# Optimization experiments

Measured on AMD Instinct MI355X. Metric: run time of the kernel, lower is better.

The kernel has to match this reference:

```python
import math
import jax, jax.numpy as jnp
import numpy as np

DIM = 2048
HID = 4 * DIM
SEQ = 2048
BATCH = 2
EPS = 1e-5


def _layernorm(x, g, b):
    mu = jnp.mean(x, axis=-1, keepdims=True)
    var = jnp.var(x, axis=-1, keepdims=True)
    return (x - mu) * jax.lax.rsqrt(var + EPS) * g + b


def setup_inputs() -> dict:
    key = jax.random.key(0)
    ks = jax.random.split(key, 12)
    s = 1.0 / math.sqrt(DIM)
    x = jax.random.normal(ks[0], (BATCH, SEQ, DIM), dtype=jnp.float32)
    # additive causal mask: 0 on/below diagonal, -1e9 above
    mask = jnp.where(jnp.tril(jnp.ones((SEQ, SEQ), dtype=bool)), 0.0, -1e9).astype(jnp.float32)
    freqs_cis = jax.random.normal(ks[1], (SEQ, 64), dtype=jnp.float32)  # unused by forward
    return {
        "x": x,
        "mask": mask,
        "start_pos": 0,
        "freqs_cis": freqs_cis,
        "wq": jax.random.normal(ks[2], (DIM, DIM), dtype=jnp.float32) * s,
        "bq": jnp.zeros((DIM,), dtype=jnp.float32),
        "wk": jax.random.normal(ks[3], (DIM, DIM), dtype=jnp.float32) * s,
        "bk": jnp.zeros((DIM,), dtype=jnp.float32),
        "wv": jax.random.normal(ks[4], (DIM, DIM), dtype=jnp.float32) * s,
        "bv": jnp.zeros((DIM,), dtype=jnp.float32),
        "g_ln1": jnp.ones((DIM,), dtype=jnp.float32),
        "b_ln1": jnp.zeros((DIM,), dtype=jnp.float32),
        "g_ln2": jnp.ones((DIM,), dtype=jnp.float32),
        "b_ln2": jnp.zeros((DIM,), dtype=jnp.float32),
        "w1": jax.random.normal(ks[5], (DIM, HID), dtype=jnp.float32) * s,
        "b1": jnp.zeros((HID,), dtype=jnp.float32),
        "w2": jax.random.normal(ks[6], (HID, DIM), dtype=jnp.float32) * (1.0 / math.sqrt(HID)),
        "b2": jnp.zeros((DIM,), dtype=jnp.float32),
    }


def reference(x, mask, start_pos, freqs_cis, wq, bq, wk, bk, wv, bv,
              g_ln1, b_ln1, g_ln2, b_ln2, w1, b1, w2, b2):
    # pre-norm attention (no head split; scale by sqrt(full dim); dropout=eval identity)
    h = _layernorm(x, g_ln1, b_ln1)
    q = h @ wq + bq
    k = h @ wk + bk
    v = h @ wv + bv
    scores = jnp.einsum('bqd,bkd->bqk', q, k) / math.sqrt(DIM) + mask
    attn = jax.nn.softmax(scores, axis=-1)
    attn_out = jnp.einsum('bqk,bkd->bqd', attn, v)
    h2 = _layernorm(x + attn_out, g_ln2, b_ln2)
    ffn = jax.nn.gelu(h2 @ w1 + b1, approximate=False) @ w2 + b2
    # NOTE: original code adds FFN output to the ORIGINAL x (attn residual dropped here)
    return x + ffn
```

## Files before the change

### kernel.cpp

```cpp
#include <hip/hip_runtime.h>
#include <math.h>

#define DIM_ 2048
#define HID_ 8192
#define SEQ_ 2048
#define BATCH_ 2
#define TOK_ (BATCH_*SEQ_)

typedef __attribute__((ext_vector_type(4))) float f32x4;
typedef __attribute__((ext_vector_type(8))) __bf16 bf16x8;
typedef __attribute__((ext_vector_type(4))) unsigned int u32x4;
typedef __attribute__((ext_vector_type(4))) short s16x4;
typedef __attribute__((ext_vector_type(8))) short s16x8;
typedef __attribute__((address_space(3))) short* lds_sp;

__device__ __forceinline__ short f2bf(float f) {
  union { float f; unsigned u; } v; v.f = f;
  unsigned r = v.u + 0x7FFFu + ((v.u >> 16) & 1u);
  return (short)(r >> 16);
}
__device__ __forceinline__ float bf2f(short s) {
  union { unsigned u; float f; } v; v.u = ((unsigned)(unsigned short)s) << 16;
  return v.f;
}

__device__ __forceinline__ f32x4 mfma16(u32x4 a, u32x4 b, f32x4 c) {
  return __builtin_amdgcn_mfma_f32_16x16x32_bf16(
      __builtin_bit_cast(bf16x8, a), __builtin_bit_cast(bf16x8, b), c, 0, 0, 0);
}

#define DSR(dst, addr) asm volatile("ds_read_b128 %0, %1" : "=v"(dst) : "v"(addr))
#define BARv()  __builtin_amdgcn_s_barrier()
#define LGKM0() do { asm volatile("s_waitcnt lgkmcnt(0)" ::: "memory"); \
                     __builtin_amdgcn_sched_barrier(0); } while(0)
#define LGKM8() asm volatile("s_waitcnt lgkmcnt(8)" ::: "memory")
#define VM6()   asm volatile("s_waitcnt vmcnt(6)" ::: "memory")
#define VM3()   asm volatile("s_waitcnt vmcnt(3)" ::: "memory")
#define PRIO1() __builtin_amdgcn_s_setprio(1)
#define PRIO0() __builtin_amdgcn_s_setprio(0)

#define TILE_MAP(BM, BN) \
  const int nwg  = gridDim.x * gridDim.y; \
  const int orig = blockIdx.y * gridDim.x + blockIdx.x; \
  const int wgid = (orig & 7) * (nwg >> 3) + (orig >> 3); \
  const int gy4  = (int)gridDim.y << 2; \
  const int rem  = wgid % gy4; \
  const int tn   = ((wgid / gy4) * 4 + (rem & 3)) * (BN); \
  const int tm   = (rem >> 2) * (BM);

template<int EPI>
__device__ __forceinline__ void epi_store(void* Cv, const float* bias, const float* aux,
                                          int z, long long sC, int ldc, int N,
                                          int row, int col, float v)
{
  if (EPI == 1) {
    ((float*)Cv + (long long)z * sC)[(long long)row * ldc + col] = v;
  } else if (EPI == 0) {
    v += bias[col];
    ((short*)Cv + (long long)z * sC)[(long long)row * ldc + col] = f2bf(v);
  } else if (EPI == 2) {
    v += bias[col];
    v = 0.5f * v * (1.0f + erff(v * 0.70710678118654752f));
    ((short*)Cv + (long long)z * sC)[(long long)row * ldc + col] = f2bf(v);
  } else if (EPI == 3) {
    v += bias[col] + aux[(long long)row * ldc + col];
    ((float*)Cv + (long long)z * sC)[(long long)row * ldc + col] = v;
  } else {
    v = v * 0.022097086912079608f + aux[(long long)row * ldc + col];
    ((short*)Cv + (long long)z * sC)[(long long)row * ldc + col] = f2bf(v);
  }
}

#define RD_A(mlo, slot) do { \
  const unsigned ab_ = aBase8 + (unsigned)(slot)*16384u + (mlo)*2048u; \
  DSR(af[0][0], ab_ + offk0);         DSR(af[0][1], ab_ + offk1); \
  DSR(af[1][0], ab_ + 2048u + offk0); DSR(af[1][1], ab_ + 2048u + offk1); \
} while(0)

#define RD_B(slot) do { \
  const unsigned bb_ = bBase8 + (unsigned)(slot)*32768u; \
  DSR(bfr[0][0], bb_ + offk0);         DSR(bfr[0][1], bb_ + offk1); \
  DSR(bfr[1][0], bb_ + 2048u + offk0); DSR(bfr[1][1], bb_ + 2048u + offk1); \
  DSR(bfr[2][0], bb_ + 4096u + offk0); DSR(bfr[2][1], bb_ + 4096u + offk1); \
  DSR(bfr[3][0], bb_ + 6144u + offk0); DSR(bfr[3][1], bb_ + 6144u + offk1); \
} while(0)

#define MM(mlo) do { \
  _Pragma("unroll") \
  for (int n_ = 0; n_ < 4; ++n_) { \
    acc[(mlo)][n_]   = mfma16(af[0][0], bfr[n_][0], acc[(mlo)][n_]); \
    acc[(mlo)][n_]   = mfma16(af[0][1], bfr[n_][1], acc[(mlo)][n_]); \
    acc[(mlo)+1][n_] = mfma16(af[1][0], bfr[n_][0], acc[(mlo)+1][n_]); \
    acc[(mlo)+1][n_] = mfma16(af[1][1], bfr[n_][1], acc[(mlo)+1][n_]); \
  } \
} while(0)

template<int EPI>
__global__ __launch_bounds__(512, 2)
void gemm8p(const short* __restrict__ A, const short* __restrict__ B,
            void* __restrict__ Cv, const float* __restrict__ bias,
            const float* __restrict__ aux,
            int M, int N, int K, int lda, int ldb, int ldc,
            long long sA, long long sB, long long sC)
{
  __shared__ __align__(16) short As[3*128*64];
  __shared__ __align__(16) short Bs[3*256*64];
  const int lane = threadIdx.x & 63;
  const int wave = threadIdx.x >> 6;
  const int wr = wave >> 2, wc = wave & 3;
  TILE_MAP(128, 256)
  const int z  = blockIdx.z;
  A += (long long)z * sA;
  B += (long long)z * sB;

  const int NT = K >> 6;

  const int lr    = lane >> 3;
  const int lrow  = wave * 8 + lr;
  const int lslot = ((lane & 7) ^ lr) << 3;
  const short* pA = A + (long long)(tm + lrow) * lda + lslot;
  const short* pB = B + (long long)(tn + lrow) * ldb + lslot;
  const long long lda64 = 64LL * lda;
  const long long ldb64 = 64LL * ldb;

  auto stageA = [&](int t, int slot) {
    const long long ko = (long long)t << 6;
    const int db = slot * 8192 + wave * 512;
    __builtin_amdgcn_global_load_lds(
        (const __attribute__((address_space(1))) void*)(pA + ko),
        (__attribute__((address_space(3))) void*)(As + db), 16, 0, 0);
    __builtin_amdgcn_global_load_lds(
        (const __attribute__((address_space(1))) void*)(pA + lda64 + ko),
        (__attribute__((address_space(3))) void*)(As + db + 4096), 16, 0, 0);
  };
  auto stageB = [&](int t, int slot) {
    const long long ko = (long long)t << 6;
    const int db = slot * 16384 + wave * 512;
    __builtin_amdgcn_global_load_lds(
        (const __attribute__((address_space(1))) void*)(pB + ko),
        (__attribute__((address_space(3))) void*)(Bs + db), 16, 0, 0);
    __builtin_amdgcn_global_load_lds(
        (const __attribute__((address_space(1))) void*)(pB + ldb64 + ko),
        (__attribute__((address_space(3))) void*)(Bs + db + 4096), 16, 0, 0);
    __builtin_amdgcn_global_load_lds(
        (const __attribute__((address_space(1))) void*)(pB + 2*ldb64 + ko),
        (__attribute__((address_space(3))) void*)(Bs + db + 8192), 16, 0, 0);
    __builtin_amdgcn_global_load_lds(
        (const __attribute__((address_space(1))) void*)(pB + 3*ldb64 + ko),
        (__attribute__((address_space(3))) void*)(Bs + db + 12288), 16, 0, 0);
  };

  const unsigned asB = (unsigned)(unsigned long long)(lds_sp)As;
  const unsigned bsB = (unsigned)(unsigned long long)(lds_sp)Bs;
  const int l15 = lane & 15, l4 = lane >> 4;
  const unsigned offk0 = (unsigned)(( l4      ^ (lane & 7)) << 4);
  const unsigned offk1 = (unsigned)(((l4 + 4) ^ (lane & 7)) << 4);
  const unsigned aBase8 = asB + (unsigned)((wr * 64 + l15) * 128);
  const unsigned bBase8 = bsB + (unsigned)((wc * 64 + l15) * 128);

  f32x4 acc[4][4] = {};
  u32x4 af[2][2], bfr[4][2];

  stageB(0, 0); stageA(0, 0);
  stageB(1 < NT ? 1 : 0, 1); stageA(1 < NT ? 1 : 0, 1);
  VM6();
  BARv();

  int rd = 0;
  #pragma unroll 1
  for (int t = 0; t < NT; ++t) {
    const int st = rd + 2 >= 3 ? rd - 1 : rd + 2;
    const int tc = t + 2 < NT ? t + 2 : NT - 1;
    RD_A(0, rd); RD_B(rd);
    stageB(tc, st);
    LGKM8();
    BARv(); LGKM0();
    PRIO1(); MM(0); PRIO0();
    BARv();
    RD_A(2, rd);
    stageA(tc, st);
    VM6();
    BARv(); LGKM0();
    PRIO1(); MM(2); PRIO0();
    BARv();
    rd = rd + 1 >= 3 ? 0 : rd + 1;
  }

  const int row0 = tm + wr * 64 + l4 * 4;
  const int col0 = tn + wc * 64 + l15;
  #pragma unroll
  for (int mi = 0; mi < 4; ++mi)
    #pragma unroll
    for (int j = 0; j < 4; ++j)
      #pragma unroll
      for (int ni = 0; ni < 4; ++ni)
        epi_store<EPI>(Cv, bias, aux, z, sC, ldc, N,
                       row0 + mi * 16 + j, col0 + ni * 16, acc[mi][ni][j]);
}

#define HRD(slot) do { \
  const unsigned a_ = aBaseH + (unsigned)(slot)*8192u; \
  const unsigned b_ = bBaseH + (unsigned)(slot)*16384u; \
  DSR(af[0], a_ + offk);          DSR(af[1], a_ + 1024u + offk); \
  DSR(af[2], a_ + 2048u + offk);  DSR(af[3], a_ + 3072u + offk); \
  DSR(bf[0], b_ + offk);          DSR(bf[1], b_ + 1024u + offk); \
  DSR(bf[2], b_ + 2048u + offk);  DSR(bf[3], b_ + 3072u + offk); \
} while(0)

#define HMM() do { \
  _Pragma("unroll") \
  for (int mi = 0; mi < 4; ++mi) \
    _Pragma("unroll") \
    for (int ni = 0; ni < 4; ++ni) \
      acc[mi][ni] = mfma16(af[mi], bf[ni], acc[mi][ni]); \
} while(0)

template<int EPI>
__global__ __launch_bounds__(512, 4)
void gemm_hi(const short* __restrict__ A, const short* __restrict__ B,
             void* __restrict__ Cv, const float* __restrict__ bias,
             const float* __restrict__ aux,
             int M, int N, int K, int lda, int ldb, int ldc,
             long long sA, long long sB, long long sC)
{
  __shared__ __align__(16) short As[3*128*32];
  __shared__ __align__(16) short Bs[3*256*32];
  const int lane = threadIdx.x & 63;
  const int wave = threadIdx.x >> 6;
  const int wr = wave >> 2, wc = wave & 3;
  TILE_MAP(128, 256)
  const int z = blockIdx.z;
  A += (long long)z * sA;
  B += (long long)z * sB;

  const int NT = K >> 5;

  const int rr   = wave * 16 + (lane >> 2);
  const int soff = (((lane & 3) ^ ((lane >> 2) & 3)) << 3);
  const short* pA = A + (long long)(tm + rr) * lda + soff;
  const short* pB = B + (long long)(tn + rr) * ldb + soff;
  const long long ldb128 = 128LL * ldb;

  auto stage = [&](int t, int slot) {
    const long long ko = (long long)t << 5;
    __builtin_amdgcn_global_load_lds(
        (const __attribute__((address_space(1))) void*)(pA + ko),
        (__attribute__((address_space(3))) void*)(As + slot * 4096 + wave * 512), 16, 0, 0);
    __builtin_amdgcn_global_load_lds(
        (const __attribute__((address_space(1))) void*)(pB + ko),
        (__attribute__((address_space(3))) void*)(Bs + slot * 8192 + wave * 512), 16, 0, 0);
    __builtin_amdgcn_global_load_lds(
        (const __attribute__((address_space(1))) void*)(pB + ldb128 + ko),
        (__attribute__((address_space(3))) void*)(Bs + slot * 8192 + 4096 + wave * 512), 16, 0, 0);
  };

  const unsigned asB = (unsigned)(unsigned long long)(lds_sp)As;
  const unsigned bsB = (unsigned)(unsigned long long)(lds_sp)Bs;
  const int l15 = lane & 15, l4 = lane >> 4;
  const unsigned offk  = (unsigned)((l4 ^ (l15 & 3)) << 4);
  const unsigned aBaseH = asB + (unsigned)(wr * 4096 + l15 * 64);
  const unsigned bBaseH = bsB + (unsigned)(wc * 4096 + l15 * 64);

  f32x4 acc[4][4] = {};
  u32x4 af[4], bf[4];

  stage(0, 0);
  stage(1 < NT ? 1 : 0, 1);
  VM3();
  BARv();

  int rd = 0;
  #pragma unroll 1
  for (int t = 0; t < NT; ++t) {
    const int st = rd + 2 >= 3 ? rd - 1 : rd + 2;
    const int tc = t + 2 < NT ? t + 2 : NT - 1;
    HRD(rd);
    stage(tc, st);
    BARv(); LGKM0();
    PRIO1(); HMM(); PRIO0();
    VM3();
    BARv();
    rd = rd + 1 >= 3 ? 0 : rd + 1;
  }

  const int row0 = tm + wr * 64 + l4 * 4;
  const int col0 = tn + wc * 64 + l15;
  #pragma unroll
  for (int mi = 0; mi < 4; ++mi)
    #pragma unroll
    for (int j = 0; j < 4; ++j)
      #pragma unroll
      for (int ni = 0; ni < 4; ++ni)
        epi_store<EPI>(Cv, bias, aux, z, sC, ldc, N,
                       row0 + mi * 16 + j, col0 + ni * 16, acc[mi][ni][j]);
}

__global__ __launch_bounds__(256)
void ln_kernel(const float* __restrict__ x, const float* __restrict__ res,
               const float* __restrict__ g, const float* __restrict__ b,
               short* __restrict__ out, int hasres)
{
  const int row = blockIdx.x;
  const int tid = threadIdx.x;
  const float4* X = (const float4*)x + (long long)row * 512;
  float4 v0 = X[tid], v1 = X[tid + 256];
  if (hasres) {
    const float4* R = (const float4*)res + (long long)row * 512;
    float4 r0 = R[tid], r1 = R[tid + 256];
    v0.x += r0.x; v0.y += r0.y; v0.z += r0.z; v0.w += r0.w;
    v1.x += r1.x; v1.y += r1.y; v1.z += r1.z; v1.w += r1.w;
  }
  float s1 = v0.x + v0.y + v0.z + v0.w + v1.x + v1.y + v1.z + v1.w;
  float s2 = v0.x*v0.x + v0.y*v0.y + v0.z*v0.z + v0.w*v0.w
           + v1.x*v1.x + v1.y*v1.y + v1.z*v1.z + v1.w*v1.w;
  #pragma unroll
  for (int o = 32; o > 0; o >>= 1) { s1 += __shfl_xor(s1, o); s2 += __shfl_xor(s2, o); }
  __shared__ float red[8];
  if ((tid & 63) == 0) { red[tid >> 6] = s1; red[4 + (tid >> 6)] = s2; }
  __syncthreads();
  s1 = red[0] + red[1] + red[2] + red[3];
  s2 = red[4] + red[5] + red[6] + red[7];
  const float mean = s1 * (1.0f / 2048.0f);
  const float var  = s2 * (1.0f / 2048.0f) - mean * mean;
  const float rstd = rsqrtf(var + 1e-5f);
  const float4* G  = (const float4*)g;
  const float4* Bb = (const float4*)b;
  float4 g0 = G[tid], g1 = G[tid + 256], b0 = Bb[tid], b1 = Bb[tid + 256];
  s16x4 o0, o1;
  o0[0] = f2bf((v0.x - mean) * rstd * g0.x + b0.x);
  o0[1] = f2bf((v0.y - mean) * rstd * g0.y + b0.y);
  o0[2] = f2bf((v0.z - mean) * rstd * g0.z + b0.z);
  o0[3] = f2bf((v0.w - mean) * rstd * g0.w + b0.w);
  o1[0] = f2bf((v1.x - mean) * rstd * g1.x + b1.x);
  o1[1] = f2bf((v1.y - mean) * rstd * g1.y + b1.y);
  o1[2] = f2bf((v1.z - mean) * rstd * g1.z + b1.z);
  o1[3] = f2bf((v1.w - mean) * rstd * g1.w + b1.w);
  *(s16x4*)&out[(long long)row * 2048 + tid * 4]        = o0;
  *(s16x4*)&out[(long long)row * 2048 + 1024 + tid * 4] = o1;
}

__global__ __launch_bounds__(256)
void softmax_bf16_kernel(short* __restrict__ probs)
{
  const long long row = blockIdx.x;
  const int tid = threadIdx.x;
  short* P = probs + row * 2048 + tid * 8;
  s16x8 in = *(const s16x8*)P;
  float a[8];
  #pragma unroll
  for (int i = 0; i < 8; ++i) a[i] = bf2f(in[i]);
  float mx = a[0];
  #pragma unroll
  for (int i = 1; i < 8; ++i) mx = fmaxf(mx, a[i]);
  #pragma unroll
  for (int o = 32; o > 0; o >>= 1) mx = fmaxf(mx, __shfl_xor(mx, o));
  __shared__ float red[8];
  if ((tid & 63) == 0) red[tid >> 6] = mx;
  __syncthreads();
  mx = fmaxf(fmaxf(red[0], red[1]), fmaxf(red[2], red[3]));
  float e[8], sum = 0.f;
  #pragma unroll
  for (int i = 0; i < 8; ++i) { e[i] = __expf(a[i] - mx); sum += e[i]; }
  #pragma unroll
  for (int o = 32; o > 0; o >>= 1) sum += __shfl_xor(sum, o);
  if ((tid & 63) == 0) red[4 + (tid >> 6)] = sum;
  __syncthreads();
  sum = red[4] + red[5] + red[6] + red[7];
  const float inv = 1.0f / sum;
  s16x8 o;
  #pragma unroll
  for (int i = 0; i < 8; ++i) o[i] = f2bf(e[i] * inv);
  *(s16x8*)P = o;
}

__global__ __launch_bounds__(256)
void cvt_transpose64(const float* __restrict__ in, short* __restrict__ out,
                     int R, int C)
{
  __shared__ float t[64][69];
  const int r0 = blockIdx.y << 6, c0 = blockIdx.x << 6;
  const int tx = threadIdx.x & 15, ty = threadIdx.x >> 4;
  #pragma unroll
  for (int p = 0; p < 4; ++p) {
    const int r = ty + p * 16;
    float4 v = *(const float4*)&in[(long long)(r0 + r) * C + c0 + tx * 4];
    t[r][tx*4+0] = v.x; t[r][tx*4+1] = v.y; t[r][tx*4+2] = v.z; t[r][tx*4+3] = v.w;
  }
  __syncthreads();
  #pragma unroll
  for (int p = 0; p < 4; ++p) {
    const int oc = ty + p * 16;
    s16x4 o;
    o[0] = f2bf(t[tx*4+0][oc]); o[1] = f2bf(t[tx*4+1][oc]);
    o[2] = f2bf(t[tx*4+2][oc]); o[3] = f2bf(t[tx*4+3][oc]);
    *(s16x4*)&out[(long long)(c0 + oc) * R + r0 + tx * 4] = o;
  }
}

__global__ __launch_bounds__(256)
void transpose_bf16_kernel(const short* __restrict__ in, short* __restrict__ out,
                           int ldin, int ldout, long long sin_, long long sout_)
{
  __shared__ short t[32][33];
  in  += (long long)blockIdx.z * sin_;
  out += (long long)blockIdx.z * sout_;
  const int tx = threadIdx.x & 31, ty = threadIdx.x >> 5;
  const int r0 = blockIdx.y << 5, c0 = blockIdx.x << 5;
  #pragma unroll
  for (int i = 0; i < 32; i += 8)
    t[ty + i][tx] = in[(long long)(r0 + ty + i) * ldin + c0 + tx];
  __syncthreads();
  #pragma unroll
  for (int i = 0; i < 32; i += 8)
    out[(long long)(c0 + ty + i) * ldout + r0 + tx] = t[tx][ty + i];
}

__global__ __launch_bounds__(256)
void concat_bias_kernel(const float* a, const float* b, const float* c, float* o)
{
  const int i = blockIdx.x * 256 + threadIdx.x;
  o[i] = i < 2048 ? a[i] : (i < 4096 ? b[i - 2048] : c[i - 4096]);
}

extern "C" void kernel_launch(void* const* d_in, const int* in_sizes, int n_in,
                              void* d_out, int out_size, void* d_ws, size_t ws_size,
                              hipStream_t stream)
{
  const float* x    = (const float*)d_in[0];
  const float* mask = (const float*)d_in[1];
  const float* wq   = (const float*)d_in[4];
  const float* bq   = (const float*)d_in[5];
  const float* wk   = (const float*)d_in[6];
  const float* bk   = (const float*)d_in[7];
  const float* wv   = (const float*)d_in[8];
  const float* bv   = (const float*)d_in[9];
  const float* g1   = (const float*)d_in[10];
  const float* b1   = (const float*)d_in[11];
  const float* g2   = (const float*)d_in[12];
  const float* b2   = (const float*)d_in[13];
  const float* w1   = (const float*)d_in[14];
  const float* bw1  = (const float*)d_in[15];
  const float* w2   = (const float*)d_in[16];
  const float* bw2  = (const float*)d_in[17];
  float* out = (float*)d_out;

  char* p = (char*)d_ws;
  auto take = [&](size_t bytes) { char* r = p; p += (bytes + 255) & ~(size_t)255; return r; };
  short* wqkvT = (short*)take((size_t)3 * DIM_ * DIM_ * 2);
  short* w1T   = (short*)take((size_t)DIM_ * HID_ * 2);
  short* w2T   = (short*)take((size_t)HID_ * DIM_ * 2);
  short* h_bf  = (short*)take((size_t)TOK_ * DIM_ * 2);
  short* qkv   = (short*)take((size_t)TOK_ * 3 * DIM_ * 2);
  short* vT    = (short*)take((size_t)BATCH_ * DIM_ * SEQ_ * 2);
  float* attno = (float*)take((size_t)TOK_ * DIM_ * 4);
  short* attn  = (short*)take((size_t)BATCH_ * SEQ_ * SEQ_ * 2);
  float* cbias = (float*)take((size_t)3 * DIM_ * 4);
  short* ffn1  = qkv;
  short* h2    = h_bf;

  const dim3 blk(256), gblk(512);
  cvt_transpose64<<<dim3(DIM_/64, DIM_/64), blk, 0, stream>>>(wq, wqkvT, DIM_, DIM_);
  cvt_transpose64<<<dim3(DIM_/64, DIM_/64), blk, 0, stream>>>(wk, wqkvT + (size_t)DIM_*DIM_, DIM_, DIM_);
  cvt_transpose64<<<dim3(DIM_/64, DIM_/64), blk, 0, stream>>>(wv, wqkvT + (size_t)2*DIM_*DIM_, DIM_, DIM_);
  cvt_transpose64<<<dim3(HID_/64, DIM_/64), blk, 0, stream>>>(w1, w1T, DIM_, HID_);
  cvt_transpose64<<<dim3(DIM_/64, HID_/64), blk, 0, stream>>>(w2, w2T, HID_, DIM_);
  concat_bias_kernel<<<24, blk, 0, stream>>>(bq, bk, bv, cbias);
  ln_kernel<<<TOK_, blk, 0, stream>>>(x, nullptr, g1, b1, h_bf, 0);
  gemm8p<0><<<dim3(6144/256, TOK_/128, 1), gblk, 0, stream>>>(
      h_bf, wqkvT, qkv, cbias, nullptr, TOK_, 6144, DIM_, DIM_, DIM_, 6144, 0, 0, 0);
  gemm8p<4><<<dim3(SEQ_/256, SEQ_/128, BATCH_), gblk, 0, stream>>>(
      qkv, qkv + DIM_, attn, nullptr, mask, SEQ_, SEQ_, DIM_, 6144, 6144, SEQ_,
      (long long)SEQ_ * 6144, (long long)SEQ_ * 6144, (long long)SEQ_ * SEQ_);
  softmax_bf16_kernel<<<BATCH_ * SEQ_, blk, 0, stream>>>(attn);
  transpose_bf16_kernel<<<dim3(DIM_/32, SEQ_/32, BATCH_), blk, 0, stream>>>(
      qkv + 2*DIM_, vT, 6144, SEQ_, (long long)SEQ_ * 6144, (long long)DIM_ * SEQ_);
  gemm8p<1><<<dim3(DIM_/256, SEQ_/128, BATCH_), gblk, 0, stream>>>(
      attn, vT, attno, nullptr, nullptr, SEQ_, DIM_, SEQ_, SEQ_, SEQ_, DIM_,
      (long long)SEQ_ * SEQ_, (long long)DIM_ * SEQ_, (long long)SEQ_ * DIM_);
  ln_kernel<<<TOK_, blk, 0, stream>>>(x, attno, g2, b2, h2, 1);
  gemm_hi<2><<<dim3(HID_/256, TOK_/128, 1), gblk, 0, stream>>>(
      h2, w1T, ffn1, bw1, nullptr, TOK_, HID_, DIM_, DIM_, DIM_, HID_, 0, 0, 0);
  gemm_hi<3><<<dim3(DIM_/256, TOK_/128, 1), gblk, 0, stream>>>(
      ffn1, w2T, out, bw2, x, TOK_, DIM_, HID_, HID_, HID_, DIM_, 0, 0, 0);
}
```

Baseline: 626.2 us.

## Replace gemm8p with gemm_hi everywhere and change its LDS swizzle

Deletes the 64-wide-K gemm8p kernel and routes the QKV, score and attn@V GEMMs through the 32-wide-K gemm_hi kernel already used for the FFN. It also changes gemm_hi's XOR swizzle, both on the store side (lane>>3 instead of lane>>2) and on the read side ((l15>>1)&3), to cut LDS bank conflicts. This unifies the GEMM path, but the smaller K tile may lower data reuse per barrier for the attention GEMMs.

Result: no change. 627.5 us (+0.2%).

```diff
diff --git a/kernel.cpp b/kernel.cpp
--- a/kernel.cpp
+++ b/kernel.cpp
@@ -33,8 +33,6 @@
 #define BARv()  __builtin_amdgcn_s_barrier()
 #define LGKM0() do { asm volatile("s_waitcnt lgkmcnt(0)" ::: "memory"); \
                      __builtin_amdgcn_sched_barrier(0); } while(0)
-#define LGKM8() asm volatile("s_waitcnt lgkmcnt(8)" ::: "memory")
-#define VM6()   asm volatile("s_waitcnt vmcnt(6)" ::: "memory")
 #define VM3()   asm volatile("s_waitcnt vmcnt(3)" ::: "memory")
 #define PRIO1() __builtin_amdgcn_s_setprio(1)
 #define PRIO0() __builtin_amdgcn_s_setprio(0)
@@ -71,133 +69,6 @@
   }
 }
 
-#define RD_A(mlo, slot) do { \
-  const unsigned ab_ = aBase8 + (unsigned)(slot)*16384u + (mlo)*2048u; \
-  DSR(af[0][0], ab_ + offk0);         DSR(af[0][1], ab_ + offk1); \
-  DSR(af[1][0], ab_ + 2048u + offk0); DSR(af[1][1], ab_ + 2048u + offk1); \
-} while(0)
-
-#define RD_B(slot) do { \
-  const unsigned bb_ = bBase8 + (unsigned)(slot)*32768u; \
-  DSR(bfr[0][0], bb_ + offk0);         DSR(bfr[0][1], bb_ + offk1); \
-  DSR(bfr[1][0], bb_ + 2048u + offk0); DSR(bfr[1][1], bb_ + 2048u + offk1); \
-  DSR(bfr[2][0], bb_ + 4096u + offk0); DSR(bfr[2][1], bb_ + 4096u + offk1); \
-  DSR(bfr[3][0], bb_ + 6144u + offk0); DSR(bfr[3][1], bb_ + 6144u + offk1); \
-} while(0)
-
-#define MM(mlo) do { \
-  _Pragma("unroll") \
-  for (int n_ = 0; n_ < 4; ++n_) { \
-    acc[(mlo)][n_]   = mfma16(af[0][0], bfr[n_][0], acc[(mlo)][n_]); \
-    acc[(mlo)][n_]   = mfma16(af[0][1], bfr[n_][1], acc[(mlo)][n_]); \
-    acc[(mlo)+1][n_] = mfma16(af[1][0], bfr[n_][0], acc[(mlo)+1][n_]); \
-    acc[(mlo)+1][n_] = mfma16(af[1][1], bfr[n_][1], acc[(mlo)+1][n_]); \
-  } \
-} while(0)
-
-template<int EPI>
-__global__ __launch_bounds__(512, 2)
-void gemm8p(const short* __restrict__ A, const short* __restrict__ B,
-            void* __restrict__ Cv, const float* __restrict__ bias,
-            const float* __restrict__ aux,
-            int M, int N, int K, int lda, int ldb, int ldc,
-            long long sA, long long sB, long long sC)
-{
-  __shared__ __align__(16) short As[3*128*64];
-  __shared__ __align__(16) short Bs[3*256*64];
-  const int lane = threadIdx.x & 63;
-  const int wave = threadIdx.x >> 6;
-  const int wr = wave >> 2, wc = wave & 3;
-  TILE_MAP(128, 256)
-  const int z  = blockIdx.z;
-  A += (long long)z * sA;
-  B += (long long)z * sB;
-
-  const int NT = K >> 6;
-
-  const int lr    = lane >> 3;
-  const int lrow  = wave * 8 + lr;
-  const int lslot = ((lane & 7) ^ lr) << 3;
-  const short* pA = A + (long long)(tm + lrow) * lda + lslot;
-  const short* pB = B + (long long)(tn + lrow) * ldb + lslot;
-  const long long lda64 = 64LL * lda;
-  const long long ldb64 = 64LL * ldb;
-
-  auto stageA = [&](int t, int slot) {
-    const long long ko = (long long)t << 6;
-    const int db = slot * 8192 + wave * 512;
-    __builtin_amdgcn_global_load_lds(
-        (const __attribute__((address_space(1))) void*)(pA + ko),
-        (__attribute__((address_space(3))) void*)(As + db), 16, 0, 0);
-    __builtin_amdgcn_global_load_lds(
-        (const __attribute__((address_space(1))) void*)(pA + lda64 + ko),
-        (__attribute__((address_space(3))) void*)(As + db + 4096), 16, 0, 0);
-  };
-  auto stageB = [&](int t, int slot) {
-    const long long ko = (long long)t << 6;
-    const int db = slot * 16384 + wave * 512;
-    __builtin_amdgcn_global_load_lds(
-        (const __attribute__((address_space(1))) void*)(pB + ko),
-        (__attribute__((address_space(3))) void*)(Bs + db), 16, 0, 0);
-    __builtin_amdgcn_global_load_lds(
-        (const __attribute__((address_space(1))) void*)(pB + ldb64 + ko),
-        (__attribute__((address_space(3))) void*)(Bs + db + 4096), 16, 0, 0);
-    __builtin_amdgcn_global_load_lds(
-        (const __attribute__((address_space(1))) void*)(pB + 2*ldb64 + ko),
-        (__attribute__((address_space(3))) void*)(Bs + db + 8192), 16, 0, 0);
-    __builtin_amdgcn_global_load_lds(
-        (const __attribute__((address_space(1))) void*)(pB + 3*ldb64 + ko),
-        (__attribute__((address_space(3))) void*)(Bs + db + 12288), 16, 0, 0);
-  };
-
-  const unsigned asB = (unsigned)(unsigned long long)(lds_sp)As;
-  const unsigned bsB = (unsigned)(unsigned long long)(lds_sp)Bs;
-  const int l15 = lane & 15, l4 = lane >> 4;
-  const unsigned offk0 = (unsigned)(( l4      ^ (lane & 7)) << 4);
-  const unsigned offk1 = (unsigned)(((l4 + 4) ^ (lane & 7)) << 4);
-  const unsigned aBase8 = asB + (unsigned)((wr * 64 + l15) * 128);
-  const unsigned bBase8 = bsB + (unsigned)((wc * 64 + l15) * 128);
-
-  f32x4 acc[4][4] = {};
-  u32x4 af[2][2], bfr[4][2];
-
-  stageB(0, 0); stageA(0, 0);
-  stageB(1 < NT ? 1 : 0, 1); stageA(1 < NT ? 1 : 0, 1);
-  VM6();
-  BARv();
-
-  int rd = 0;
-  #pragma unroll 1
-  for (int t = 0; t < NT; ++t) {
-    const int st = rd + 2 >= 3 ? rd - 1 : rd + 2;
-    const int tc = t + 2 < NT ? t + 2 : NT - 1;
-    RD_A(0, rd); RD_B(rd);
-    stageB(tc, st);
-    LGKM8();
-    BARv(); LGKM0();
-    PRIO1(); MM(0); PRIO0();
-    BARv();
-    RD_A(2, rd);
-    stageA(tc, st);
-    VM6();
-    BARv(); LGKM0();
-    PRIO1(); MM(2); PRIO0();
-    BARv();
-    rd = rd + 1 >= 3 ? 0 : rd + 1;
-  }
-
-  const int row0 = tm + wr * 64 + l4 * 4;
-  const int col0 = tn + wc * 64 + l15;
-  #pragma unroll
-  for (int mi = 0; mi < 4; ++mi)
-    #pragma unroll
-    for (int j = 0; j < 4; ++j)
-      #pragma unroll
-      for (int ni = 0; ni < 4; ++ni)
-        epi_store<EPI>(Cv, bias, aux, z, sC, ldc, N,
-                       row0 + mi * 16 + j, col0 + ni * 16, acc[mi][ni][j]);
-}
-
 #define HRD(slot) do { \
   const unsigned a_ = aBaseH + (unsigned)(slot)*8192u; \
   const unsigned b_ = bBaseH + (unsigned)(slot)*16384u; \
@@ -236,7 +107,7 @@
   const int NT = K >> 5;
 
   const int rr   = wave * 16 + (lane >> 2);
-  const int soff = (((lane & 3) ^ ((lane >> 2) & 3)) << 3);
+  const int soff = (((lane & 3) ^ ((lane >> 3) & 3)) << 3);
   const short* pA = A + (long long)(tm + rr) * lda + soff;
   const short* pB = B + (long long)(tn + rr) * ldb + soff;
   const long long ldb128 = 128LL * ldb;
@@ -257,7 +128,7 @@
   const unsigned asB = (unsigned)(unsigned long long)(lds_sp)As;
   const unsigned bsB = (unsigned)(unsigned long long)(lds_sp)Bs;
   const int l15 = lane & 15, l4 = lane >> 4;
-  const unsigned offk  = (unsigned)((l4 ^ (l15 & 3)) << 4);
+  const unsigned offk  = (unsigned)((l4 ^ ((l15 >> 1) & 3)) << 4);
   const unsigned aBaseH = asB + (unsigned)(wr * 4096 + l15 * 64);
   const unsigned bBaseH = bsB + (unsigned)(wc * 4096 + l15 * 64);
 
@@ -466,15 +337,15 @@
   cvt_transpose64<<<dim3(DIM_/64, HID_/64), blk, 0, stream>>>(w2, w2T, HID_, DIM_);
   concat_bias_kernel<<<24, blk, 0, stream>>>(bq, bk, bv, cbias);
   ln_kernel<<<TOK_, blk, 0, stream>>>(x, nullptr, g1, b1, h_bf, 0);
-  gemm8p<0><<<dim3(6144/256, TOK_/128, 1), gblk, 0, stream>>>(
+  gemm_hi<0><<<dim3(6144/256, TOK_/128, 1), gblk, 0, stream>>>(
       h_bf, wqkvT, qkv, cbias, nullptr, TOK_, 6144, DIM_, DIM_, DIM_, 6144, 0, 0, 0);
-  gemm8p<4><<<dim3(SEQ_/256, SEQ_/128, BATCH_), gblk, 0, stream>>>(
+  gemm_hi<4><<<dim3(SEQ_/256, SEQ_/128, BATCH_), gblk, 0, stream>>>(
       qkv, qkv + DIM_, attn, nullptr, mask, SEQ_, SEQ_, DIM_, 6144, 6144, SEQ_,
       (long long)SEQ_ * 6144, (long long)SEQ_ * 6144, (long long)SEQ_ * SEQ_);
   softmax_bf16_kernel<<<BATCH_ * SEQ_, blk, 0, stream>>>(attn);
   transpose_bf16_kernel<<<dim3(DIM_/32, SEQ_/32, BATCH_), blk, 0, stream>>>(
       qkv + 2*DIM_, vT, 6144, SEQ_, (long long)SEQ_ * 6144, (long long)DIM_ * SEQ_);
-  gemm8p<1><<<dim3(DIM_/256, SEQ_/128, BATCH_), gblk, 0, stream>>>(
+  gemm_hi<1><<<dim3(DIM_/256, SEQ_/128, BATCH_), gblk, 0, stream>>>(
       attn, vT, attno, nullptr, nullptr, SEQ_, DIM_, SEQ_, SEQ_, SEQ_, DIM_,
       (long long)SEQ_ * SEQ_, (long long)DIM_ * SEQ_, (long long)SEQ_ * DIM_);
   ln_kernel<<<TOK_, blk, 0, stream>>>(x, attno, g2, b2, h2, 1);
```
